# Performance work log

Measured on AMD Instinct MI355X. Metric: run time of the kernel, lower is better.

The kernel has to match this reference:

```python
import jax, jax.numpy as jnp
import numpy as np


def _mlp(x, W1, b1, W2, b2, W3, b3, W4, b4, W5, b5):
    # x: [..., 3] -> [..., 12]
    h = jax.nn.silu(x @ W1 + b1)
    h = jax.nn.silu(h @ W2 + b2)
    h = jax.nn.silu(h @ W3 + b3)
    h = jax.nn.silu(h @ W4 + b4)
    return h @ W5 + b5


def setup_inputs() -> dict:
    key = jax.random.key(0)
    ks = jax.random.split(key, 11)
    N = 1_000_000
    s = lambda k, shp, fan: jax.random.normal(k, shp, dtype=jnp.float32) * (1.0 / np.sqrt(fan))
    return {
        "x": jax.random.normal(ks[0], (N, 3), dtype=jnp.float32),
        "W1": s(ks[1], (3, 64), 3), "b1": jnp.zeros((64,), jnp.float32),
        "W2": s(ks[2], (64, 64), 64), "b2": jnp.zeros((64,), jnp.float32),
        "W3": s(ks[3], (64, 64), 64), "b3": jnp.zeros((64,), jnp.float32),
        "W4": s(ks[4], (64, 64), 64), "b4": jnp.zeros((64,), jnp.float32),
        "W5": s(ks[5], (64, 12), 64), "b5": jnp.zeros((12,), jnp.float32),
    }


def reference(x, W1, b1, W2, b2, W3, b3, W4, b4, W5, b5):
    # Full Jacobian d field / d x per point, via 3 fused forward-mode (JVP) passes
    # (input dim 3 < output dim 12, so forward mode is optimal).
    N = x.shape[0]
    f = lambda xx: _mlp(xx, W1, b1, W2, b2, W3, b3, W4, b4, W5, b5)
    eye = jnp.eye(3, dtype=x.dtype)

    def jvp_dir(t):  # t: [3] basis direction
        return jax.jvp(f, (x,), (jnp.broadcast_to(t, x.shape),))[1]  # [N, 12]

    jac = jax.vmap(jvp_dir)(eye)             # [3(partial), N, 12]
    jac = jnp.transpose(jac, (1, 0, 2))      # [N, partialxyz=3, 12]
    # 12 -> (xyz=3, reim=2, eb=2), matching einops rearrange 'n p (xyz reim eb)'
    return jac.reshape(N, 3, 3, 2, 2)
```

## Files before the change

kernel.cpp:

```cpp
#include <hip/hip_runtime.h>
#include <hip/hip_bf16.h>


#define THREADS 256

typedef float  f32x16 __attribute__((ext_vector_type(16)));
typedef float  f32x4  __attribute__((ext_vector_type(4)));
typedef short  s16x8  __attribute__((ext_vector_type(8)));

#define MFMA(a, b, c) __builtin_amdgcn_mfma_f32_32x32x16_bf16(a, b, c, 0, 0, 0)

__device__ __forceinline__ uint cvtpk(float a, float b) {
    uint r;
    asm("v_cvt_pk_bf16_f32 %0, %1, %2" : "=v"(r) : "v"(a), "v"(b));
    return r;
}
__device__ __forceinline__ void plswap(uint &a, uint &b) {
    asm("v_permlane32_swap_b32 %0, %1" : "+v"(a), "+v"(b));
}
__device__ __forceinline__ float quad0(float v) {
    return __int_as_float(__builtin_amdgcn_mov_dpp(__float_as_int(v), 0, 0xF, 0xF, false));
}
__device__ __forceinline__ ushort bfhi(float v) {
    uint u = __float_as_uint(v);
    return (ushort)((u + 0x7FFFu + ((u >> 16) & 1u)) >> 16);
}
__device__ __forceinline__ s16x8 mk8(uint a, uint b, uint c, uint d) {
    union { uint u[4]; s16x8 s; } x;
    x.u[0] = a; x.u[1] = b; x.u[2] = c; x.u[3] = d;
    return x.s;
}
__device__ __forceinline__ void pack_pairs(const f32x16 &A, const int i0,
                                           uint (&H)[4], uint (&L)[4]) {
    #pragma unroll
    for (int q = 0; q < 4; ++q) {
        float v0 = A[i0 + 2 * q], v1 = A[i0 + 2 * q + 1];
        uint  Hc = cvtpk(v0, v1);
        float r0 = v0 - __uint_as_float(Hc << 16);
        float r1 = v1 - __uint_as_float(Hc & 0xFFFF0000u);
        H[q] = Hc;
        L[q] = cvtpk(r0, r1);
    }
    plswap(H[0], H[2]); plswap(H[1], H[3]);
    plswap(L[0], L[2]); plswap(L[1], L[3]);
}

__global__ __launch_bounds__(THREADS, 3)
void PartialDerivatives_mfma(const float* __restrict__ x,
                             const float* __restrict__ W1, const float* __restrict__ b1,
                             const float* __restrict__ W2, const float* __restrict__ b2,
                             const float* __restrict__ W3, const float* __restrict__ b3,
                             const float* __restrict__ W4, const float* __restrict__ b4,
                             const float* __restrict__ W5,
                             float* __restrict__ out, int N, int ntiles)
{
    __shared__ __align__(16) ushort sWH[3 * 2 * 4 * 64 * 8];
    __shared__ __align__(16) ushort sW1[2 * 64 * 8];
    __shared__ __align__(16) ushort sW5[4 * 64 * 8];
    __shared__ __align__(16) float  sB[4 * 64];

    const int tid = threadIdx.x;
    for (int i = tid; i < 12288; i += THREADS) {
        int e = i & 7, lane = (i >> 3) & 63, kk = (i >> 9) & 3, mt = (i >> 11) & 1, l = i >> 12;
        int n = mt * 32 + (lane & 31);
        int k = kk * 16 + (lane >> 5) * 8 + e;
        const float* W = (l == 0) ? W2 : (l == 1) ? W3 : W4;
        sWH[i] = bfhi(W[k * 64 + n]);
    }
    for (int i = tid; i < 1024; i += THREADS) {
        int e = i & 7, lane = (i >> 3) & 63, mt = i >> 9;
        int n = mt * 32 + (lane & 31);
        int k = (lane >> 5) * 8 + e;
        sW1[i] = (k < 3) ? bfhi(W1[k * 64 + n]) : (ushort)0;
    }
    for (int i = tid; i < 2048; i += THREADS) {
        int e = i & 7, lane = (i >> 3) & 63, kk = i >> 9;
        int m = lane & 31;
        int k = kk * 16 + (lane >> 5) * 8 + e;
        sW5[i] = (m < 12) ? bfhi(W5[k * 12 + m]) : (ushort)0;
    }
    if (tid < 64) {
        sB[tid] = b1[tid]; sB[64 + tid] = b2[tid];
        sB[128 + tid] = b3[tid]; sB[192 + tid] = b4[tid];
    }
    __syncthreads();

    const int  lane = tid & 63;
    const int  hi   = lane >> 5;
    const int  s    = lane & 3;
    const bool is0  = (s == 0);
    const int  pq   = (lane & 31) >> 2;

    const int wid = blockIdx.x * (THREADS / 64) + (tid >> 6);
    const int nw  = gridDim.x * (THREADS / 64);

#define SILU16(A)                                                              \
    { _Pragma("unroll")                                                        \
      for (int i = 0; i < 16; ++i) {                                           \
          float v  = A[i];                                                     \
          float zb = quad0(v);                                                 \
          float ez = __expf(-zb);                                              \
          float sg = __builtin_amdgcn_rcpf(1.f + ez);                          \
          float d  = __builtin_fmaf(zb * sg, 1.f - sg, sg);                    \
          A[i] = v * (is0 ? sg : d);                                           \
      } }

#define EPILOGUE()                                                             \
    {   SILU16(a00); SILU16(a01); SILU16(a10); SILU16(a11);                    \
        pack_pairs(a00, 0, Bh[0][0], Bl[0][0]);                                \
        pack_pairs(a01, 0, Bh[0][1], Bl[0][1]);                                \
        pack_pairs(a00, 8, Bh[1][0], Bl[1][0]);                                \
        pack_pairs(a01, 8, Bh[1][1], Bl[1][1]);                                \
        pack_pairs(a10, 0, Bh[2][0], Bl[2][0]);                                \
        pack_pairs(a11, 0, Bh[2][1], Bl[2][1]);                                \
        pack_pairs(a10, 8, Bh[3][0], Bl[3][0]);                                \
        pack_pairs(a11, 8, Bh[3][1], Bl[3][1]); }

#define BINIT(boff)                                                            \
    { _Pragma("unroll")                                                        \
      for (int q = 0; q < 4; ++q) {                                            \
          f32x4 bb0 = *(const f32x4*)&sB[(boff) + q * 8 + hi * 4];             \
          f32x4 bb1 = *(const f32x4*)&sB[(boff) + 32 + q * 8 + hi * 4];        \
          _Pragma("unroll")                                                    \
          for (int j = 0; j < 4; ++j) {                                        \
              a00[q * 4 + j] = bb0[j]; a01[q * 4 + j] = bb0[j];                \
              a10[q * 4 + j] = bb1[j]; a11[q * 4 + j] = bb1[j];                \
          } } }

#define HSTEP(l, kk)                                                           \
    {   s16x8 A0 = *(const s16x8*)&sWH[(((l) * 2 + 0) * 4 + (kk)) * 512 + lane * 8]; \
        s16x8 A1 = *(const s16x8*)&sWH[(((l) * 2 + 1) * 4 + (kk)) * 512 + lane * 8]; \
        s16x8 bh0 = mk8(Bh[kk][0][0], Bh[kk][0][1], Bh[kk][0][2], Bh[kk][0][3]);     \
        s16x8 bl0 = mk8(Bl[kk][0][0], Bl[kk][0][1], Bl[kk][0][2], Bl[kk][0][3]);     \
        s16x8 bh1 = mk8(Bh[kk][1][0], Bh[kk][1][1], Bh[kk][1][2], Bh[kk][1][3]);     \
        s16x8 bl1 = mk8(Bl[kk][1][0], Bl[kk][1][1], Bl[kk][1][2], Bl[kk][1][3]);     \
        a00 = MFMA(A0, bh0, a00); a00 = MFMA(A0, bl0, a00);                    \
        a01 = MFMA(A0, bh1, a01); a01 = MFMA(A0, bl1, a01);                    \
        a10 = MFMA(A1, bh0, a10); a10 = MFMA(A1, bl0, a10);                    \
        a11 = MFMA(A1, bh1, a11); a11 = MFMA(A1, bl1, a11); }

    #pragma unroll 1
    for (int t = wid; t < ntiles; t += nw) {
        const int base = t * 16;
        f32x16 a00, a01, a10, a11;
        uint Bh[4][2][4], Bl[4][2][4];

        BINIT(0);
        {
            uint b1h[2][2] = {{0u,0u},{0u,0u}}, b1l[2][2] = {{0u,0u},{0u,0u}};
            #pragma unroll
            for (int nt = 0; nt < 2; ++nt) {
                if (hi == 0) {
                    if (is0) {
                        int pt = base + nt * 8 + pq;
                        if (pt > N - 1) pt = N - 1;
                        const float* xp = x + (size_t)pt * 3;
                        float x0 = xp[0], x1 = xp[1], x2 = xp[2];
                        uint H0 = cvtpk(x0, x1);
                        uint H1 = cvtpk(x2, 0.f);
                        float r0 = x0 - __uint_as_float(H0 << 16);
                        float r1 = x1 - __uint_as_float(H0 & 0xFFFF0000u);
                        float r2 = x2 - __uint_as_float(H1 << 16);
                        b1h[nt][0] = H0; b1h[nt][1] = H1;
                        b1l[nt][0] = cvtpk(r0, r1); b1l[nt][1] = cvtpk(r2, 0.f);
                    } else {
                        b1h[nt][0] = (s == 1) ? 0x3F80u : (s == 2) ? 0x3F800000u : 0u;
                        b1h[nt][1] = (s == 3) ? 0x3F80u : 0u;
                    }
                }
            }
            s16x8 A0 = *(const s16x8*)&sW1[0 * 512 + lane * 8];
            s16x8 A1 = *(const s16x8*)&sW1[1 * 512 + lane * 8];
            s16x8 bh0 = mk8(b1h[0][0], b1h[0][1], 0u, 0u);
            s16x8 bl0 = mk8(b1l[0][0], b1l[0][1], 0u, 0u);
            s16x8 bh1 = mk8(b1h[1][0], b1h[1][1], 0u, 0u);
            s16x8 bl1 = mk8(b1l[1][0], b1l[1][1], 0u, 0u);
            a00 = MFMA(A0, bh0, a00); a00 = MFMA(A0, bl0, a00);
            a01 = MFMA(A0, bh1, a01); a01 = MFMA(A0, bl1, a01);
            a10 = MFMA(A1, bh0, a10); a10 = MFMA(A1, bl0, a10);
            a11 = MFMA(A1, bh1, a11); a11 = MFMA(A1, bl1, a11);
        }
        EPILOGUE();

        #pragma unroll 1
        for (int l = 0; l < 3; ++l) {
            BINIT((l + 1) * 64);
            HSTEP(l, 0); HSTEP(l, 1); HSTEP(l, 2); HSTEP(l, 3);
            EPILOGUE();
        }

        f32x16 o0, o1;
        #pragma unroll
        for (int i = 0; i < 16; ++i) { o0[i] = 0.f; o1[i] = 0.f; }
        #pragma unroll
        for (int kk = 0; kk < 4; ++kk) {
            s16x8 A5 = *(const s16x8*)&sW5[kk * 512 + lane * 8];
            s16x8 bh0 = mk8(Bh[kk][0][0], Bh[kk][0][1], Bh[kk][0][2], Bh[kk][0][3]);
            s16x8 bl0 = mk8(Bl[kk][0][0], Bl[kk][0][1], Bl[kk][0][2], Bl[kk][0][3]);
            s16x8 bh1 = mk8(Bh[kk][1][0], Bh[kk][1][1], Bh[kk][1][2], Bh[kk][1][3]);
            s16x8 bl1 = mk8(Bl[kk][1][0], Bl[kk][1][1], Bl[kk][1][2], Bl[kk][1][3]);
            o0 = MFMA(A5, bh0, o0); o0 = MFMA(A5, bl0, o0);
            o1 = MFMA(A5, bh1, o1); o1 = MFMA(A5, bl1, o1);
        }

        if (!is0) {
            const int row = s - 1;
            #pragma unroll
            for (int nt = 0; nt < 2; ++nt) {
                int pt = base + nt * 8 + pq;
                if (pt < N) {
                    float* ob = out + (size_t)pt * 36 + row * 12;
                    const f32x16 &O = nt ? o1 : o0;
                    if (hi == 0) {
                        *(f32x4*)(ob + 0) = (f32x4){O[0], O[1], O[2], O[3]};
                        *(f32x4*)(ob + 8) = (f32x4){O[4], O[5], O[6], O[7]};
                    } else {
                        *(f32x4*)(ob + 4) = (f32x4){O[0], O[1], O[2], O[3]};
                    }
                }
            }
        }
    }
#undef SILU16
#undef EPILOGUE
#undef BINIT
#undef HSTEP
}

extern "C" void kernel_launch(void* const* d_in, const int* in_sizes, int n_in,
                              void* d_out, int out_size, void* d_ws, size_t ws_size,
                              hipStream_t stream) {
    const float* x  = (const float*)d_in[0];
    const float* W1 = (const float*)d_in[1];
    const float* b1 = (const float*)d_in[2];
    const float* W2 = (const float*)d_in[3];
    const float* b2 = (const float*)d_in[4];
    const float* W3 = (const float*)d_in[5];
    const float* b3 = (const float*)d_in[6];
    const float* W4 = (const float*)d_in[7];
    const float* b4 = (const float*)d_in[8];
    const float* W5 = (const float*)d_in[9];
    float* out = (float*)d_out;

    const int N = in_sizes[0] / 3;
    const int ntiles = (N + 15) / 16;
    const int blocks = 2048;
    PartialDerivatives_mfma<<<blocks, THREADS, 0, stream>>>(
        x, W1, b1, W2, b2, W3, b3, W4, b4, W5, out, N, ntiles);
}
```

Measured before the change: 648.5 us.

## Replace SiLU with LDS lookup table and split tiles to cut register pressure

Swaps the exp/rcp computation of SiLU and its derivative for linear interpolation in a 513-entry shared-memory table over [-10,10], with clamping outside that range. Restructures the per-tile work so each 8-point sub-tile runs through the layers separately, halving live accumulators, and raises the launch-bounds occupancy hint from 3 to 4. The table approximation brings interpolation error and clamps large inputs, where the derivative term z*sigmoid*(1-sigmoid) is cut off. Processing the sub-tiles one after another also gives each MFMA chain less independent work to interleave.

```diff
diff --git a/kernel.cpp b/kernel.cpp
--- a/kernel.cpp
+++ b/kernel.cpp
@@ -45,7 +45,7 @@
     plswap(L[0], L[2]); plswap(L[1], L[3]);
 }
 
-__global__ __launch_bounds__(THREADS, 3)
+__global__ __launch_bounds__(THREADS, 4)
 void PartialDerivatives_mfma(const float* __restrict__ x,
                              const float* __restrict__ W1, const float* __restrict__ b1,
                              const float* __restrict__ W2, const float* __restrict__ b2,
@@ -58,6 +58,7 @@
     __shared__ __align__(16) ushort sW1[2 * 64 * 8];
     __shared__ __align__(16) ushort sW5[4 * 64 * 8];
     __shared__ __align__(16) float  sB[4 * 64];
+    __shared__ __align__(8)  float2 sTab[2][513];
 
     const int tid = threadIdx.x;
     for (int i = tid; i < 12288; i += THREADS) {
@@ -83,6 +84,17 @@
         sB[tid] = b1[tid]; sB[64 + tid] = b2[tid];
         sB[128 + tid] = b3[tid]; sB[192 + tid] = b4[tid];
     }
+    for (int i = tid; i < 1026; i += THREADS) {
+        int  c  = (i >= 513);
+        int  k  = c ? i - 513 : i;
+        float z0 = -10.f + k * 0.0390625f;
+        float z1 = z0 + 0.0390625f;
+        float s0 = 1.f / (1.f + __expf(-z0));
+        float s1 = 1.f / (1.f + __expf(-z1));
+        float y0 = c ? s0 * (1.f + z0 * (1.f - s0)) : s0;
+        float y1 = c ? s1 * (1.f + z1 * (1.f - s1)) : s1;
+        sTab[c][k] = make_float2(y0, y1 - y0);
+    }
     __syncthreads();
 
     const int  lane = tid & 63;
@@ -90,6 +102,7 @@
     const int  s    = lane & 3;
     const bool is0  = (s == 0);
     const int  pq   = (lane & 31) >> 2;
+    const float2* __restrict__ tb = &sTab[is0 ? 0 : 1][0];
 
     const int wid = blockIdx.x * (THREADS / 64) + (tid >> 6);
     const int nw  = gridDim.x * (THREADS / 64);
@@ -97,134 +110,116 @@
 #define SILU16(A)                                                              \
     { _Pragma("unroll")                                                        \
       for (int i = 0; i < 16; ++i) {                                           \
-          float v  = A[i];                                                     \
-          float zb = quad0(v);                                                 \
-          float ez = __expf(-zb);                                              \
-          float sg = __builtin_amdgcn_rcpf(1.f + ez);                          \
-          float d  = __builtin_fmaf(zb * sg, 1.f - sg, sg);                    \
-          A[i] = v * (is0 ? sg : d);                                           \
+          float zb = quad0(A[i]);                                              \
+          float zc = fminf(fmaxf(zb, -10.f), 10.f);                            \
+          float u  = __builtin_fmaf(zc, 25.6f, 256.0f);                        \
+          float fl = floorf(u);                                                \
+          float fr = u - fl;                                                   \
+          float2 e = tb[(int)fl];                                              \
+          A[i] *= __builtin_fmaf(e.y, fr, e.x);                                \
       } }
 
-#define EPILOGUE()                                                             \
-    {   SILU16(a00); SILU16(a01); SILU16(a10); SILU16(a11);                    \
-        pack_pairs(a00, 0, Bh[0][0], Bl[0][0]);                                \
-        pack_pairs(a01, 0, Bh[0][1], Bl[0][1]);                                \
-        pack_pairs(a00, 8, Bh[1][0], Bl[1][0]);                                \
-        pack_pairs(a01, 8, Bh[1][1], Bl[1][1]);                                \
-        pack_pairs(a10, 0, Bh[2][0], Bl[2][0]);                                \
-        pack_pairs(a11, 0, Bh[2][1], Bl[2][1]);                                \
-        pack_pairs(a10, 8, Bh[3][0], Bl[3][0]);                                \
-        pack_pairs(a11, 8, Bh[3][1], Bl[3][1]); }
-
-#define BINIT(boff)                                                            \
+#define EPILOGUE_NT(nt, aLo, aHi)                                              \
+    {   SILU16(aLo); SILU16(aHi);                                              \
+        pack_pairs(aLo, 0, Bh[0][nt], Bl[0][nt]);                              \
+        pack_pairs(aLo, 8, Bh[1][nt], Bl[1][nt]);                              \
+        pack_pairs(aHi, 0, Bh[2][nt], Bl[2][nt]);                              \
+        pack_pairs(aHi, 8, Bh[3][nt], Bl[3][nt]); }
+
+#define BINIT(boff, aLo, aHi)                                                  \
     { _Pragma("unroll")                                                        \
       for (int q = 0; q < 4; ++q) {                                            \
           f32x4 bb0 = *(const f32x4*)&sB[(boff) + q * 8 + hi * 4];             \
           f32x4 bb1 = *(const f32x4*)&sB[(boff) + 32 + q * 8 + hi * 4];        \
           _Pragma("unroll")                                                    \
           for (int j = 0; j < 4; ++j) {                                        \
-              a00[q * 4 + j] = bb0[j]; a01[q * 4 + j] = bb0[j];                \
-              a10[q * 4 + j] = bb1[j]; a11[q * 4 + j] = bb1[j];                \
+              aLo[q * 4 + j] = bb0[j]; aHi[q * 4 + j] = bb1[j];                \
           } } }
-
-#define HSTEP(l, kk)                                                           \
-    {   s16x8 A0 = *(const s16x8*)&sWH[(((l) * 2 + 0) * 4 + (kk)) * 512 + lane * 8]; \
-        s16x8 A1 = *(const s16x8*)&sWH[(((l) * 2 + 1) * 4 + (kk)) * 512 + lane * 8]; \
-        s16x8 bh0 = mk8(Bh[kk][0][0], Bh[kk][0][1], Bh[kk][0][2], Bh[kk][0][3]);     \
-        s16x8 bl0 = mk8(Bl[kk][0][0], Bl[kk][0][1], Bl[kk][0][2], Bl[kk][0][3]);     \
-        s16x8 bh1 = mk8(Bh[kk][1][0], Bh[kk][1][1], Bh[kk][1][2], Bh[kk][1][3]);     \
-        s16x8 bl1 = mk8(Bl[kk][1][0], Bl[kk][1][1], Bl[kk][1][2], Bl[kk][1][3]);     \
-        a00 = MFMA(A0, bh0, a00); a00 = MFMA(A0, bl0, a00);                    \
-        a01 = MFMA(A0, bh1, a01); a01 = MFMA(A0, bl1, a01);                    \
-        a10 = MFMA(A1, bh0, a10); a10 = MFMA(A1, bl0, a10);                    \
-        a11 = MFMA(A1, bh1, a11); a11 = MFMA(A1, bl1, a11); }
 
     #pragma unroll 1
     for (int t = wid; t < ntiles; t += nw) {
         const int base = t * 16;
-        f32x16 a00, a01, a10, a11;
         uint Bh[4][2][4], Bl[4][2][4];
 
-        BINIT(0);
-        {
-            uint b1h[2][2] = {{0u,0u},{0u,0u}}, b1l[2][2] = {{0u,0u},{0u,0u}};
+        #pragma unroll
+        for (int nt = 0; nt < 2; ++nt) {
+            f32x16 aLo, aHi;
+            BINIT(0, aLo, aHi);
+            uint h0 = 0u, h1 = 0u, l0 = 0u, l1 = 0u;
+            if (hi == 0) {
+                if (is0) {
+                    int pt = base + nt * 8 + pq;
+                    if (pt > N - 1) pt = N - 1;
+                    const float* xp = x + (size_t)pt * 3;
+                    float x0 = xp[0], x1 = xp[1], x2 = xp[2];
+                    h0 = cvtpk(x0, x1);
+                    h1 = cvtpk(x2, 0.f);
+                    float r0 = x0 - __uint_as_float(h0 << 16);
+                    float r1 = x1 - __uint_as_float(h0 & 0xFFFF0000u);
+                    float r2 = x2 - __uint_as_float(h1 << 16);
+                    l0 = cvtpk(r0, r1); l1 = cvtpk(r2, 0.f);
+                } else {
+                    h0 = (s == 1) ? 0x3F80u : (s == 2) ? 0x3F800000u : 0u;
+                    h1 = (s == 3) ? 0x3F80u : 0u;
+                }
+            }
+            s16x8 A0  = *(const s16x8*)&sW1[0 * 512 + lane * 8];
+            s16x8 A1  = *(const s16x8*)&sW1[1 * 512 + lane * 8];
+            s16x8 bh  = mk8(h0, h1, 0u, 0u);
+            s16x8 bl  = mk8(l0, l1, 0u, 0u);
+            aLo = MFMA(A0, bh, aLo); aLo = MFMA(A0, bl, aLo);
+            aHi = MFMA(A1, bh, aHi); aHi = MFMA(A1, bl, aHi);
+            EPILOGUE_NT(nt, aLo, aHi);
+        }
+
+        #pragma unroll 1
+        for (int l = 0; l < 3; ++l) {
             #pragma unroll
             for (int nt = 0; nt < 2; ++nt) {
-                if (hi == 0) {
-                    if (is0) {
-                        int pt = base + nt * 8 + pq;
-                        if (pt > N - 1) pt = N - 1;
-                        const float* xp = x + (size_t)pt * 3;
-                        float x0 = xp[0], x1 = xp[1], x2 = xp[2];
-                        uint H0 = cvtpk(x0, x1);
-                        uint H1 = cvtpk(x2, 0.f);
-                        float r0 = x0 - __uint_as_float(H0 << 16);
-                        float r1 = x1 - __uint_as_float(H0 & 0xFFFF0000u);
-                        float r2 = x2 - __uint_as_float(H1 << 16);
-                        b1h[nt][0] = H0; b1h[nt][1] = H1;
-                        b1l[nt][0] = cvtpk(r0, r1); b1l[nt][1] = cvtpk(r2, 0.f);
+                f32x16 aLo, aHi;
+                BINIT((l + 1) * 64, aLo, aHi);
+                #pragma unroll
+                for (int kk = 0; kk < 4; ++kk) {
+                    s16x8 A0 = *(const s16x8*)&sWH[((l * 2 + 0) * 4 + kk) * 512 + lane * 8];
+                    s16x8 A1 = *(const s16x8*)&sWH[((l * 2 + 1) * 4 + kk) * 512 + lane * 8];
+                    s16x8 bh = mk8(Bh[kk][nt][0], Bh[kk][nt][1], Bh[kk][nt][2], Bh[kk][nt][3]);
+                    s16x8 bl = mk8(Bl[kk][nt][0], Bl[kk][nt][1], Bl[kk][nt][2], Bl[kk][nt][3]);
+                    aLo = MFMA(A0, bh, aLo); aLo = MFMA(A0, bl, aLo);
+                    aHi = MFMA(A1, bh, aHi); aHi = MFMA(A1, bl, aHi);
+                }
+                EPILOGUE_NT(nt, aLo, aHi);
+            }
+        }
+
+        #pragma unroll
+        for (int nt = 0; nt < 2; ++nt) {
+            f32x16 o;
+            #pragma unroll
+            for (int i = 0; i < 16; ++i) o[i] = 0.f;
+            #pragma unroll
+            for (int kk = 0; kk < 4; ++kk) {
+                s16x8 A5 = *(const s16x8*)&sW5[kk * 512 + lane * 8];
+                s16x8 bh = mk8(Bh[kk][nt][0], Bh[kk][nt][1], Bh[kk][nt][2], Bh[kk][nt][3]);
+                s16x8 bl = mk8(Bl[kk][nt][0], Bl[kk][nt][1], Bl[kk][nt][2], Bl[kk][nt][3]);
+                o = MFMA(A5, bh, o); o = MFMA(A5, bl, o);
+            }
+            if (!is0) {
+                int pt = base + nt * 8 + pq;
+                if (pt < N) {
+                    float* ob = out + (size_t)pt * 36 + (s - 1) * 12;
+                    if (hi == 0) {
+                        *(f32x4*)(ob + 0) = (f32x4){o[0], o[1], o[2], o[3]};
+                        *(f32x4*)(ob + 8) = (f32x4){o[4], o[5], o[6], o[7]};
                     } else {
-                        b1h[nt][0] = (s == 1) ? 0x3F80u : (s == 2) ? 0x3F800000u : 0u;
-                        b1h[nt][1] = (s == 3) ? 0x3F80u : 0u;
+                        *(f32x4*)(ob + 4) = (f32x4){o[0], o[1], o[2], o[3]};
                     }
                 }
             }
-            s16x8 A0 = *(const s16x8*)&sW1[0 * 512 + lane * 8];
-            s16x8 A1 = *(const s16x8*)&sW1[1 * 512 + lane * 8];
-            s16x8 bh0 = mk8(b1h[0][0], b1h[0][1], 0u, 0u);
-            s16x8 bl0 = mk8(b1l[0][0], b1l[0][1], 0u, 0u);
-            s16x8 bh1 = mk8(b1h[1][0], b1h[1][1], 0u, 0u);
-            s16x8 bl1 = mk8(b1l[1][0], b1l[1][1], 0u, 0u);
-            a00 = MFMA(A0, bh0, a00); a00 = MFMA(A0, bl0, a00);
-            a01 = MFMA(A0, bh1, a01); a01 = MFMA(A0, bl1, a01);
-            a10 = MFMA(A1, bh0, a10); a10 = MFMA(A1, bl0, a10);
-            a11 = MFMA(A1, bh1, a11); a11 = MFMA(A1, bl1, a11);
         }
-        EPILOGUE();
-
-        #pragma unroll 1
-        for (int l = 0; l < 3; ++l) {
-            BINIT((l + 1) * 64);
-            HSTEP(l, 0); HSTEP(l, 1); HSTEP(l, 2); HSTEP(l, 3);
-            EPILOGUE();
-        }
-
-        f32x16 o0, o1;
-        #pragma unroll
-        for (int i = 0; i < 16; ++i) { o0[i] = 0.f; o1[i] = 0.f; }
-        #pragma unroll
-        for (int kk = 0; kk < 4; ++kk) {
-            s16x8 A5 = *(const s16x8*)&sW5[kk * 512 + lane * 8];
-            s16x8 bh0 = mk8(Bh[kk][0][0], Bh[kk][0][1], Bh[kk][0][2], Bh[kk][0][3]);
-            s16x8 bl0 = mk8(Bl[kk][0][0], Bl[kk][0][1], Bl[kk][0][2], Bl[kk][0][3]);
-            s16x8 bh1 = mk8(Bh[kk][1][0], Bh[kk][1][1], Bh[kk][1][2], Bh[kk][1][3]);
-            s16x8 bl1 = mk8(Bl[kk][1][0], Bl[kk][1][1], Bl[kk][1][2], Bl[kk][1][3]);
-            o0 = MFMA(A5, bh0, o0); o0 = MFMA(A5, bl0, o0);
-            o1 = MFMA(A5, bh1, o1); o1 = MFMA(A5, bl1, o1);
-        }
-
-        if (!is0) {
-            const int row = s - 1;
-            #pragma unroll
-            for (int nt = 0; nt < 2; ++nt) {
-                int pt = base + nt * 8 + pq;
-                if (pt < N) {
-                    float* ob = out + (size_t)pt * 36 + row * 12;
-                    const f32x16 &O = nt ? o1 : o0;
-                    if (hi == 0) {
-                        *(f32x4*)(ob + 0) = (f32x4){O[0], O[1], O[2], O[3]};
-                        *(f32x4*)(ob + 8) = (f32x4){O[4], O[5], O[6], O[7]};
-                    } else {
-                        *(f32x4*)(ob + 4) = (f32x4){O[0], O[1], O[2], O[3]};
-                    }
-                }
-            }
-        }
     }
 #undef SILU16
-#undef EPILOGUE
+#undef EPILOGUE_NT
 #undef BINIT
-#undef HSTEP
 }
 
 extern "C" void kernel_launch(void* const* d_in, const int* in_sizes, int n_in,
```

Result: slower. 684.8 us (+5.6%).
